# Performance work log

Measured on AMD Instinct MI355X. Metric: run time of the kernel, lower is better.

Reference implementation:

```python
import jax, jax.numpy as jnp
import numpy as np

B, T, D1, D2, DM, V, K = 2, 512, 256, 128, 1024, 32000, 4
SCALE = 0.05  # keep tanh/sigmoid out of full saturation with randn params


def setup_inputs() -> dict:
    key = jax.random.key(0)
    ks = jax.random.split(key, 7)
    s = lambda k, shape: SCALE * jax.random.normal(k, shape, dtype=jnp.float32)
    return {
        "gc": jax.random.normal(ks[0], (B, T, D1), dtype=jnp.float32),
        "H": s(ks[1], (K, DM, D1)),
        "U": s(ks[2], (K, D2, D1)),
        "v": s(ks[3], (V, D2)),
        "u": s(ks[4], (K, D1)),
        "b": s(ks[5], (V, K)),
        "emb": s(ks[6], (V, DM)),
    }


def reference(gc, H, U, v, u, b, emb):
    # gc: (B,T,D1)
    hc = jnp.tanh(jnp.einsum('kdi,bti->btkd', H, gc))        # (B,T,K,DM)
    tU = jnp.tanh(jnp.einsum('kji,bti->btkj', U, gc))        # (B,T,K,D2)
    # token- and context-dependent gate logits: (B,T,V,K)
    lc = (jnp.einsum('vj,btkj->btvk', v, tU)
          + jnp.einsum('ki,bti->btk', u, gc)[:, :, None, :]
          + b[None, None])
    gamma = jax.nn.sigmoid(lc[..., :K - 1])                  # (B,T,V,3)
    g0, g1, g2 = gamma[..., 0], gamma[..., 1], gamma[..., 2]
    # sigmoid-tree mixture priors: (B,T,V,K)
    pi = jnp.stack([g0 * g1, g0 * (1.0 - g1),
                    (1.0 - g0) * g2, (1.0 - g0) * (1.0 - g2)], axis=-1)
    # contract hc with embeddings per gate FIRST (avoids btikj blow-up),
    # then weight by pi -- same math as the original pi (x) emb outer product.
    dots = jnp.einsum('btkd,vd->btvk', hc, emb)              # (B,T,V,K)
    logits = jnp.sum(pi * dots, axis=-1)                     # (B,T,V)
    return jax.nn.softmax(logits, axis=-1)
```

## Files before the change

### kernel.cpp

```cpp
#include <hip/hip_runtime.h>
#include <math.h>

namespace {

typedef _Float16 f16;
typedef _Float16 f16x8 __attribute__((ext_vector_type(8)));
typedef float    f32x4 __attribute__((ext_vector_type(4)));

constexpr int kBT = 1024, kD1 = 256, kD2 = 128, kDM = 1024, kV = 32000, kK = 4;
constexpr int AR = kBT * kK;
constexpr int ROWS_H = kK * kDM;
constexpr int ROWS_U = kK * kD2;
constexpr int ROWS_ALL = ROWS_H + ROWS_U + kK;
constexpr int SLICES = 8;
constexpr int SLICE_ROWS = (ROWS_ALL + SLICES - 1) / SLICES;
constexpr int NBY = kV / 128;

__global__ __launch_bounds__(256) void prep_gemm(
    const float* __restrict__ gc, const float* __restrict__ Hm,
    const float* __restrict__ Um, const float* __restrict__ um,
    f16* __restrict__ hc, f16* __restrict__ tu, float* __restrict__ ug)
{
    __shared__ float sgc[8][kD1];
    const int btBase = blockIdx.x * 8;
    for (int idx = threadIdx.x; idx < 8 * kD1; idx += 256)
        sgc[idx / kD1][idx % kD1] = gc[(size_t)btBase * kD1 + idx];
    __syncthreads();

    const int rStart = blockIdx.y * SLICE_ROWS;
    int rEnd = rStart + SLICE_ROWS;
    if (rEnd > ROWS_ALL) rEnd = ROWS_ALL;
    for (int r = rStart + (int)threadIdx.x; r < rEnd; r += 256) {
        const float* wrow;
        if (r < ROWS_H)               wrow = Hm + (size_t)r * kD1;
        else if (r < ROWS_H + ROWS_U) wrow = Um + (size_t)(r - ROWS_H) * kD1;
        else                          wrow = um + (size_t)(r - ROWS_H - ROWS_U) * kD1;

        float acc[8] = {0.f,0.f,0.f,0.f,0.f,0.f,0.f,0.f};
        for (int i = 0; i < kD1; i += 4) {
            const float4 w = *reinterpret_cast<const float4*>(wrow + i);
            #pragma unroll
            for (int b = 0; b < 8; ++b) {
                const float4 g = *reinterpret_cast<const float4*>(&sgc[b][i]);
                acc[b] = fmaf(w.x, g.x, acc[b]);
                acc[b] = fmaf(w.y, g.y, acc[b]);
                acc[b] = fmaf(w.z, g.z, acc[b]);
                acc[b] = fmaf(w.w, g.w, acc[b]);
            }
        }
        #pragma unroll
        for (int b = 0; b < 8; ++b) {
            const int bt = btBase + b;
            if (r < ROWS_H) {
                const int k = r >> 10, d = r & 1023;
                hc[((size_t)(bt * kK + k) << 10) + d] = (f16)tanhf(acc[b]);
            } else if (r < ROWS_H + ROWS_U) {
                const int r2 = r - ROWS_H;
                const int k = r2 >> 7, j = r2 & 127;
                tu[(size_t)(bt * kK + k) * kD2 + j] = (f16)tanhf(acc[b]);
            } else {
                ug[bt * kK + (r - ROWS_H - ROWS_U)] = acc[b];
            }
        }
    }
}

__global__ __launch_bounds__(256) void cvt_kernel(
    const float* __restrict__ src, f16* __restrict__ dst, int n8)
{
    const int i = blockIdx.x * 256 + threadIdx.x;
    if (i >= n8) return;
    const float4 x0 = *reinterpret_cast<const float4*>(src + (size_t)i * 8);
    const float4 x1 = *reinterpret_cast<const float4*>(src + (size_t)i * 8 + 4);
    union { f16 h[8]; uint4 v; } u;
    u.h[0] = (f16)x0.x; u.h[1] = (f16)x0.y; u.h[2] = (f16)x0.z; u.h[3] = (f16)x0.w;
    u.h[4] = (f16)x1.x; u.h[5] = (f16)x1.y; u.h[6] = (f16)x1.z; u.h[7] = (f16)x1.w;
    *reinterpret_cast<uint4*>(dst + (size_t)i * 8) = u.v;
}

__device__ __forceinline__ uint packf16x2(float a, float b) {
    union { f16 h[2]; uint u; } z;
    z.h[0] = (f16)a; z.h[1] = (f16)b;
    return z.u;
}

__global__ __launch_bounds__(256, 2) void fused_mfma(
    const f16* __restrict__ hc,  const f16* __restrict__ tu,
    const f16* __restrict__ v16, const f16* __restrict__ e16,
    const float* __restrict__ ug, const float* __restrict__ bmat,
    float* __restrict__ out, float* __restrict__ psum)
{
    __shared__ __align__(16) f16 sA[2][128 * 64];
    __shared__ __align__(16) f16 sB[2][128 * 64];

    const int tid  = threadIdx.x;
    const int lane = tid & 63;
    const int wave = tid >> 6;
    const int fr = lane & 15, fq = lane >> 4;
    const int wrow = wave >> 1, wcol = wave & 1;
    const int aRowBase = blockIdx.x * 128;
    const int vBase    = blockIdx.y * 128;
    const int btB      = blockIdx.x * 32 + wrow * 16;

    const int srow = lane >> 3;
    const int scol = ((lane & 7) ^ srow) * 8;

    const f16* gApt = tu  + (size_t)(aRowBase + wave * 32 + srow) * kD2 + scol;
    const f16* gBpt = v16 + (size_t)(vBase    + wave * 32 + srow) * kD2 + scol;
    const f16* sApt = hc  + (size_t)(aRowBase + wave * 32 + srow) * kDM + scol;
    const f16* sBpt = e16 + (size_t)(vBase    + wave * 32 + srow) * kDM + scol;

    f16* dA = &sA[0][0] + wave * 4 * 512;
    f16* dB = &sB[0][0] + wave * 4 * 512;

#define GLD(SRC, DST)                                                         \
    __builtin_amdgcn_global_load_lds(                                         \
        (const __attribute__((address_space(1))) void*)(SRC),                 \
        (__attribute__((address_space(3))) void*)(DST), 16, 0, 0)

    auto stage_gate = [&](int t) {
        #pragma unroll
        for (int i = 0; i < 4; ++i) {
            GLD(gApt + t * 64 + i * 8 * kD2, dA + t * 8192 + i * 512);
            GLD(gBpt + t * 64 + i * 8 * kD2, dB + t * 8192 + i * 512);
        }
    };
    auto stage_dots = [&](int buf) {
        #pragma unroll
        for (int i = 0; i < 4; ++i) {
            GLD(sApt + i * 8 * kDM, dA + buf * 8192 + i * 512);
            GLD(sBpt + i * 8 * kDM, dB + buf * 8192 + i * 512);
        }
        sApt += 64; sBpt += 64;
    };

    const int ps0 = (fq ^ (fr & 7)) * 8;
    const int ps1 = ((4 + fq) ^ (fr & 7)) * 8;
    const f16* rA0 = &sA[0][0] + (wrow * 64 + fr) * 64 + ps0;
    const f16* rA1 = &sA[0][0] + (wrow * 64 + fr) * 64 + ps1;
    const f16* rB0 = &sB[0][0] + (wcol * 64 + fr) * 64 + ps0;
    const f16* rB1 = &sB[0][0] + (wcol * 64 + fr) * 64 + ps1;

    auto mmStep = [&](f32x4 (&acc)[4][4], int q) {
        const int qo = q * 8192;
        {
            f16x8 a[4], b[4];
            #pragma unroll
            for (int m = 0; m < 4; ++m)
                a[m] = *reinterpret_cast<const f16x8*>(rA0 + qo + m * 1024);
            #pragma unroll
            for (int n = 0; n < 4; ++n)
                b[n] = *reinterpret_cast<const f16x8*>(rB0 + qo + n * 1024);
            __builtin_amdgcn_s_setprio(1);
            #pragma unroll
            for (int m = 0; m < 4; ++m)
                #pragma unroll
                for (int n = 0; n < 4; ++n)
                    acc[m][n] = __builtin_amdgcn_mfma_f32_16x16x32_f16(
                        a[m], b[n], acc[m][n], 0, 0, 0);
            __builtin_amdgcn_s_setprio(0);
        }
        {
            f16x8 a[4], b[4];
            #pragma unroll
            for (int m = 0; m < 4; ++m)
                a[m] = *reinterpret_cast<const f16x8*>(rA1 + qo + m * 1024);
            #pragma unroll
            for (int n = 0; n < 4; ++n)
                b[n] = *reinterpret_cast<const f16x8*>(rB1 + qo + n * 1024);
            __builtin_amdgcn_s_setprio(1);
            #pragma unroll
            for (int m = 0; m < 4; ++m)
                #pragma unroll
                for (int n = 0; n < 4; ++n)
                    acc[m][n] = __builtin_amdgcn_mfma_f32_16x16x32_f16(
                        a[m], b[n], acc[m][n], 0, 0, 0);
            __builtin_amdgcn_s_setprio(0);
        }
    };

#define WAITBAR(VM)                                                           \
    asm volatile("s_waitcnt vmcnt(" VM ")" ::: "memory");                     \
    __builtin_amdgcn_s_barrier();                                             \
    asm volatile("" ::: "memory");
#define ENDBAR                                                                \
    asm volatile("" ::: "memory");                                            \
    __builtin_amdgcn_s_barrier();                                             \
    asm volatile("" ::: "memory");

    const f32x4 zz = {0.f, 0.f, 0.f, 0.f};

    f32x4 gacc[4][4];
    #pragma unroll
    for (int m = 0; m < 4; ++m)
        #pragma unroll
        for (int n = 0; n < 4; ++n) gacc[m][n] = zz;

    stage_gate(0);
    stage_gate(1);          WAITBAR("8")  mmStep(gacc, 0);  ENDBAR
    stage_dots(0);          WAITBAR("8")  mmStep(gacc, 1);  ENDBAR

    uint pi01[4][4], pi23[4][4];
    {
        float4 bb[4];
        #pragma unroll
        for (int n = 0; n < 4; ++n)
            bb[n] = *reinterpret_cast<const float4*>(
                bmat + (size_t)(vBase + wcol * 64 + n * 16 + fr) * 4);
        #pragma unroll
        for (int m = 0; m < 4; ++m) {
            const float4 ugv = *reinterpret_cast<const float4*>(
                ug + (btB + m * 4 + fq) * 4);
            #pragma unroll
            for (int n = 0; n < 4; ++n) {
                const float l0 = gacc[m][n][0] + ugv.x + bb[n].x;
                const float l1 = gacc[m][n][1] + ugv.y + bb[n].y;
                const float l2 = gacc[m][n][2] + ugv.z + bb[n].z;
                const float g0 = 1.f / (1.f + __expf(-l0));
                const float g1 = 1.f / (1.f + __expf(-l1));
                const float g2 = 1.f / (1.f + __expf(-l2));
                pi01[m][n] = packf16x2(g0 * g1, g0 * (1.f - g1));
                pi23[m][n] = packf16x2((1.f - g0) * g2, (1.f - g0) * (1.f - g2));
            }
        }
    }

    f32x4 dacc[4][4];
    #pragma unroll
    for (int m = 0; m < 4; ++m)
        #pragma unroll
        for (int n = 0; n < 4; ++n) dacc[m][n] = zz;

    for (int it = 0; it < 7; ++it) {
        stage_dots(1);      WAITBAR("8")  mmStep(dacc, 0);  ENDBAR
        stage_dots(0);      WAITBAR("8")  mmStep(dacc, 1);  ENDBAR
    }
    stage_dots(1);          WAITBAR("8")  mmStep(dacc, 0);  ENDBAR
                            WAITBAR("0")  mmStep(dacc, 1);
#undef WAITBAR
#undef ENDBAR
#undef GLD

    #pragma unroll
    for (int m = 0; m < 4; ++m) {
        const int bt = btB + m * 4 + fq;
        float es = 0.f;
        #pragma unroll
        for (int n = 0; n < 4; ++n) {
            const int v = vBase + wcol * 64 + n * 16 + fr;
            union { uint u; f16 h[2]; } p01, p23;
            p01.u = pi01[m][n]; p23.u = pi23[m][n];
            const float lg = (float)p01.h[0] * dacc[m][n][0]
                           + (float)p01.h[1] * dacc[m][n][1]
                           + (float)p23.h[0] * dacc[m][n][2]
                           + (float)p23.h[1] * dacc[m][n][3];
            out[(size_t)bt * kV + v] = lg;
            es += __expf(lg);
        }
        es += __shfl_xor(es, 1);
        es += __shfl_xor(es, 2);
        es += __shfl_xor(es, 4);
        es += __shfl_xor(es, 8);
        if (fr == 0)
            psum[(size_t)bt * 512 + blockIdx.y * 2 + wcol] = es;
    }
}

__global__ __launch_bounds__(256) void softmax_kernel(
    float* __restrict__ out, const float* __restrict__ psum)
{
    __shared__ float red[4];
    const int bt = blockIdx.x;
    float* row = out + (size_t)bt * kV;
    const int tid = threadIdx.x;

    float s = 0.f;
    for (int i = tid; i < 2 * NBY; i += 256) s += psum[(size_t)bt * 512 + i];
    #pragma unroll
    for (int o = 1; o < 64; o <<= 1) s += __shfl_xor(s, o);
    if ((tid & 63) == 0) red[tid >> 6] = s;
    __syncthreads();
    s = red[0] + red[1] + red[2] + red[3];
    const float inv = 1.f / s;

    for (int i = tid * 4; i < kV; i += 1024) {
        const float4 x = *reinterpret_cast<const float4*>(row + i);
        float4 y;
        y.x = __expf(x.x) * inv;
        y.y = __expf(x.y) * inv;
        y.z = __expf(x.z) * inv;
        y.w = __expf(x.w) * inv;
        *reinterpret_cast<float4*>(row + i) = y;
    }
}

}

extern "C" void kernel_launch(void* const* d_in, const int* in_sizes, int n_in,
                              void* d_out, int out_size, void* d_ws, size_t ws_size,
                              hipStream_t stream)
{
    (void)in_sizes; (void)n_in; (void)out_size; (void)ws_size;
    const float* gc   = (const float*)d_in[0];
    const float* Hm   = (const float*)d_in[1];
    const float* Um   = (const float*)d_in[2];
    const float* vmat = (const float*)d_in[3];
    const float* um   = (const float*)d_in[4];
    const float* bmat = (const float*)d_in[5];
    const float* emb  = (const float*)d_in[6];
    float* out = (float*)d_out;

    size_t off = 0;
    auto take = [&](size_t bytes) -> char* {
        char* p = (char*)d_ws + off;
        off += (bytes + 255) & ~(size_t)255;
        return p;
    };
    f16*   hc   = (f16*)  take((size_t)AR * kDM * 2);
    f16*   tu   = (f16*)  take((size_t)AR * kD2 * 2);
    f16*   v16  = (f16*)  take((size_t)kV * kD2 * 2);
    f16*   e16  = (f16*)  take((size_t)kV * kDM * 2);
    float* ug   = (float*)take((size_t)AR * 4);
    float* psum = (float*)take((size_t)kBT * 512 * 4);

    prep_gemm<<<dim3(kBT / 8, SLICES), 256, 0, stream>>>(gc, Hm, Um, um, hc, tu, ug);
    cvt_kernel<<<(kV * kD2 / 8 + 255) / 256, 256, 0, stream>>>(vmat, v16, kV * kD2 / 8);
    cvt_kernel<<<(kV * kDM / 8 + 255) / 256, 256, 0, stream>>>(emb, e16, kV * kDM / 8);
    fused_mfma<<<dim3(AR / 128, NBY), 256, 0, stream>>>(
        hc, tu, v16, e16, ug, bmat, out, psum);
    softmax_kernel<<<dim3(kBT), 256, 0, stream>>>(out, psum);
}
```

Baseline: 531.2 us.

## Load B operand directly from global into registers, bypassing LDS

The B tile (v16/e16 rows) is no longer staged through shared memory. Each wave now loads its MFMA B fragments straight from global memory into a register double-buffer (B0/B1), and the vmcnt waits are raised to cover the extra outstanding loads. This halves LDS use and removes the B-side LDS reads, but each B row is now fetched by both wave rows rather than shared, and register pressure grows under launch_bounds(256,2). Ordering also depends on vmcnt counting, which may not match how the compiler schedules the register loads.

Measured after the change: 799.6 us. 1.51x slower.

```diff
diff --git a/kernel.cpp b/kernel.cpp
--- a/kernel.cpp
+++ b/kernel.cpp
@@ -91,7 +91,6 @@
     float* __restrict__ out, float* __restrict__ psum)
 {
     __shared__ __align__(16) f16 sA[2][128 * 64];
-    __shared__ __align__(16) f16 sB[2][128 * 64];
 
     const int tid  = threadIdx.x;
     const int lane = tid & 63;
@@ -105,32 +104,42 @@
     const int srow = lane >> 3;
     const int scol = ((lane & 7) ^ srow) * 8;
 
-    const f16* gApt = tu  + (size_t)(aRowBase + wave * 32 + srow) * kD2 + scol;
-    const f16* gBpt = v16 + (size_t)(vBase    + wave * 32 + srow) * kD2 + scol;
-    const f16* sApt = hc  + (size_t)(aRowBase + wave * 32 + srow) * kDM + scol;
-    const f16* sBpt = e16 + (size_t)(vBase    + wave * 32 + srow) * kDM + scol;
+    const f16* gApt = tu + (size_t)(aRowBase + wave * 32 + srow) * kD2 + scol;
+    const f16* sApt = hc + (size_t)(aRowBase + wave * 32 + srow) * kDM + scol;
+
+    const f16* gBpt = v16 + (size_t)(vBase + wcol * 64 + fr) * kD2 + fq * 8;
+    const f16* sBpt = e16 + (size_t)(vBase + wcol * 64 + fr) * kDM + fq * 8;
 
     f16* dA = &sA[0][0] + wave * 4 * 512;
-    f16* dB = &sB[0][0] + wave * 4 * 512;
 
 #define GLD(SRC, DST)                                                         \
     __builtin_amdgcn_global_load_lds(                                         \
         (const __attribute__((address_space(1))) void*)(SRC),                 \
         (__attribute__((address_space(3))) void*)(DST), 16, 0, 0)
 
-    auto stage_gate = [&](int t) {
-        #pragma unroll
-        for (int i = 0; i < 4; ++i) {
+    f16x8 B0[8], B1[8];
+
+    auto stage_gate = [&](int t, f16x8 (&Bq)[8]) {
+        #pragma unroll
+        for (int i = 0; i < 4; ++i)
             GLD(gApt + t * 64 + i * 8 * kD2, dA + t * 8192 + i * 512);
-            GLD(gBpt + t * 64 + i * 8 * kD2, dB + t * 8192 + i * 512);
-        }
+        #pragma unroll
+        for (int kk = 0; kk < 2; ++kk)
+            #pragma unroll
+            for (int n = 0; n < 4; ++n)
+                Bq[kk * 4 + n] = *reinterpret_cast<const f16x8*>(
+                    gBpt + t * 64 + (size_t)n * 16 * kD2 + kk * 32);
     };
-    auto stage_dots = [&](int buf) {
-        #pragma unroll
-        for (int i = 0; i < 4; ++i) {
+    auto stage_dots = [&](int buf, f16x8 (&Bq)[8]) {
+        #pragma unroll
+        for (int i = 0; i < 4; ++i)
             GLD(sApt + i * 8 * kDM, dA + buf * 8192 + i * 512);
-            GLD(sBpt + i * 8 * kDM, dB + buf * 8192 + i * 512);
-        }
+        #pragma unroll
+        for (int kk = 0; kk < 2; ++kk)
+            #pragma unroll
+            for (int n = 0; n < 4; ++n)
+                Bq[kk * 4 + n] = *reinterpret_cast<const f16x8*>(
+                    sBpt + (size_t)n * 16 * kDM + kk * 32);
         sApt += 64; sBpt += 64;
     };
 
@@ -138,43 +147,35 @@
     const int ps1 = ((4 + fq) ^ (fr & 7)) * 8;
     const f16* rA0 = &sA[0][0] + (wrow * 64 + fr) * 64 + ps0;
     const f16* rA1 = &sA[0][0] + (wrow * 64 + fr) * 64 + ps1;
-    const f16* rB0 = &sB[0][0] + (wcol * 64 + fr) * 64 + ps0;
-    const f16* rB1 = &sB[0][0] + (wcol * 64 + fr) * 64 + ps1;
-
-    auto mmStep = [&](f32x4 (&acc)[4][4], int q) {
+
+    auto mmStep = [&](f32x4 (&acc)[4][4], int q, const f16x8 (&Bq)[8]) {
         const int qo = q * 8192;
         {
-            f16x8 a[4], b[4];
+            f16x8 a[4];
             #pragma unroll
             for (int m = 0; m < 4; ++m)
                 a[m] = *reinterpret_cast<const f16x8*>(rA0 + qo + m * 1024);
-            #pragma unroll
-            for (int n = 0; n < 4; ++n)
-                b[n] = *reinterpret_cast<const f16x8*>(rB0 + qo + n * 1024);
             __builtin_amdgcn_s_setprio(1);
             #pragma unroll
             for (int m = 0; m < 4; ++m)
                 #pragma unroll
                 for (int n = 0; n < 4; ++n)
                     acc[m][n] = __builtin_amdgcn_mfma_f32_16x16x32_f16(
-                        a[m], b[n], acc[m][n], 0, 0, 0);
+                        a[m], Bq[n], acc[m][n], 0, 0, 0);
             __builtin_amdgcn_s_setprio(0);
         }
         {
-            f16x8 a[4], b[4];
+            f16x8 a[4];
             #pragma unroll
             for (int m = 0; m < 4; ++m)
                 a[m] = *reinterpret_cast<const f16x8*>(rA1 + qo + m * 1024);
-            #pragma unroll
-            for (int n = 0; n < 4; ++n)
-                b[n] = *reinterpret_cast<const f16x8*>(rB1 + qo + n * 1024);
             __builtin_amdgcn_s_setprio(1);
             #pragma unroll
             for (int m = 0; m < 4; ++m)
                 #pragma unroll
                 for (int n = 0; n < 4; ++n)
                     acc[m][n] = __builtin_amdgcn_mfma_f32_16x16x32_f16(
-                        a[m], b[n], acc[m][n], 0, 0, 0);
+                        a[m], Bq[4 + n], acc[m][n], 0, 0, 0);
             __builtin_amdgcn_s_setprio(0);
         }
     };
@@ -196,9 +197,9 @@
         #pragma unroll
         for (int n = 0; n < 4; ++n) gacc[m][n] = zz;
 
-    stage_gate(0);
-    stage_gate(1);          WAITBAR("8")  mmStep(gacc, 0);  ENDBAR
-    stage_dots(0);          WAITBAR("8")  mmStep(gacc, 1);  ENDBAR
+    stage_gate(0, B0);
+    stage_gate(1, B1);      WAITBAR("12")  mmStep(gacc, 0, B0);  ENDBAR
+    stage_dots(0, B0);      WAITBAR("12")  mmStep(gacc, 1, B1);  ENDBAR
 
     uint pi01[4][4], pi23[4][4];
     {
@@ -232,11 +233,11 @@
         for (int n = 0; n < 4; ++n) dacc[m][n] = zz;
 
     for (int it = 0; it < 7; ++it) {
-        stage_dots(1);      WAITBAR("8")  mmStep(dacc, 0);  ENDBAR
-        stage_dots(0);      WAITBAR("8")  mmStep(dacc, 1);  ENDBAR
-    }
-    stage_dots(1);          WAITBAR("8")  mmStep(dacc, 0);  ENDBAR
-                            WAITBAR("0")  mmStep(dacc, 1);
+        stage_dots(1, B1);  WAITBAR("12")  mmStep(dacc, 0, B0);  ENDBAR
+        stage_dots(0, B0);  WAITBAR("12")  mmStep(dacc, 1, B1);  ENDBAR
+    }
+    stage_dots(1, B1);      WAITBAR("12")  mmStep(dacc, 0, B0);  ENDBAR
+                            WAITBAR("0")   mmStep(dacc, 1, B1);
 #undef WAITBAR
 #undef ENDBAR
 #undef GLD
```
